# Kernel tuning notes

Measured on AMD Instinct MI355X. Metric: run time of the kernel, lower is better.

## Reference

```python
import jax, jax.numpy as jnp
import numpy as np

DIM = 512
NUM_HEADS = 8
HEAD_DIM = DIM // NUM_HEADS


def setup_inputs() -> dict:
    key = jax.random.key(0)
    k_x, k_qkv, k_p = jax.random.split(key, 3)
    b, n, c = 8, 4096, DIM
    x = jax.random.normal(k_x, (b, n, c), dtype=jnp.float32)
    # xavier_uniform for Linear(dim, 3*dim): limit = sqrt(6/(in+out))
    lim_qkv = float(np.sqrt(6.0 / (c + 3 * c)))
    w_qkv = jax.random.uniform(k_qkv, (c, 3 * c), dtype=jnp.float32, minval=-lim_qkv, maxval=lim_qkv)
    b_qkv = jnp.zeros((3 * c,), dtype=jnp.float32)
    lim_p = float(np.sqrt(6.0 / (c + c)))
    w_p = jax.random.uniform(k_p, (c, c), dtype=jnp.float32, minval=-lim_p, maxval=lim_p)
    b_p = jnp.zeros((c,), dtype=jnp.float32)
    temperature = jnp.full((NUM_HEADS, 1, 1), 1.0 / np.sqrt(HEAD_DIM), dtype=jnp.float32)
    return {"x": x, "w_qkv": w_qkv, "b_qkv": b_qkv, "w_p": w_p, "b_p": b_p,
            "temperature": temperature}


def reference(x, w_qkv, b_qkv, w_p, b_p, temperature):
    b, n, c = x.shape
    h, d = NUM_HEADS, HEAD_DIM
    qkv = x @ w_qkv + b_qkv                      # [b, n, 3c]
    q, k, v = jnp.split(qkv, 3, axis=-1)         # each [b, n, c]
    # -> [b, h, n, d]
    q = q.reshape(b, n, h, d).transpose(0, 2, 1, 3)
    k = k.reshape(b, n, h, d).transpose(0, 2, 1, 3)
    v = v.reshape(b, n, h, d).transpose(0, 2, 1, 3)
    # channel attention: d x d score matrix, reduced over tokens n
    scores = jnp.einsum('bhnd,bhne->bhde', q, k) * temperature  # [b,h,d,d]
    attn = jax.nn.softmax(scores, axis=-1)
    # y = attn @ v^T then permute -> [b, n, h, d]
    y = jnp.einsum('bhde,bhne->bnhd', attn, v).reshape(b, n, c)
    return y @ w_p + b_p
```

## Files before the change

kernel.cpp:

```cpp
#include <hip/hip_runtime.h>

typedef __attribute__((ext_vector_type(8))) short s16x8;
typedef __attribute__((ext_vector_type(4))) short s16x4;
typedef __attribute__((ext_vector_type(4))) float fx4;

__device__ inline unsigned short f2bf(float f) {
  unsigned u = __float_as_uint(f);
  u += 0x7fffu + ((u >> 16) & 1u);
  return (unsigned short)(u >> 16);
}
__device__ inline float bf2f(unsigned short s) {
  return __uint_as_float(((unsigned)s) << 16);
}

#define GLDS16(gp, lp) \
  __builtin_amdgcn_global_load_lds((const __attribute__((address_space(1))) void*)(gp), \
                                   (__attribute__((address_space(3))) void*)(lp), 16, 0, 0)

__global__ __launch_bounds__(256) void cast_x_k(const float* __restrict__ x,
                                                unsigned short* __restrict__ xb,
                                                unsigned short* __restrict__ xT,
                                                float* __restrict__ s_part) {
  __shared__ unsigned short lt[64 * 66];
  __shared__ float red[64 * 4];
  int blk = blockIdx.x;
  int b = blk >> 9, r = blk & 511, nt = r >> 3, ct = r & 7;
  int n0 = nt * 64, c0 = ct * 64;
  int t = threadIdx.x;
  int rn = t >> 2, seg = (t & 3) * 16;
  const float* xp = x + ((size_t)b * 4096 + n0 + rn) * 512 + c0 + seg;
  fx4 v0 = *(const fx4*)&xp[0], v1 = *(const fx4*)&xp[4];
  fx4 v2 = *(const fx4*)&xp[8], v3 = *(const fx4*)&xp[12];
  unsigned short h[16];
  h[0]=f2bf(v0[0]); h[1]=f2bf(v0[1]); h[2]=f2bf(v0[2]); h[3]=f2bf(v0[3]);
  h[4]=f2bf(v1[0]); h[5]=f2bf(v1[1]); h[6]=f2bf(v1[2]); h[7]=f2bf(v1[3]);
  h[8]=f2bf(v2[0]); h[9]=f2bf(v2[1]); h[10]=f2bf(v2[2]); h[11]=f2bf(v2[3]);
  h[12]=f2bf(v3[0]); h[13]=f2bf(v3[1]); h[14]=f2bf(v3[2]); h[15]=f2bf(v3[3]);
  unsigned short* xbo = xb + ((size_t)b * 4096 + n0 + rn) * 512 + c0 + seg;
  *(s16x8*)&xbo[0] = *(s16x8*)&h[0];
  *(s16x8*)&xbo[8] = *(s16x8*)&h[8];
#pragma unroll
  for (int k = 0; k < 16; ++k) lt[(seg + k) * 66 + rn] = h[k];
  __syncthreads();
  {
    int c = t & 63, q = t >> 6;
    float p = 0.f;
#pragma unroll
    for (int i = 0; i < 16; ++i) p += bf2f(lt[c * 66 + q * 16 + i]);
    red[c * 4 + q] = p;
  }
  __syncthreads();
  if (t < 64) {
    float s = red[t * 4] + red[t * 4 + 1] + red[t * 4 + 2] + red[t * 4 + 3];
    s_part[((size_t)(b * 64 + nt)) * 512 + c0 + t] = s;
  }
  int c = t >> 2, nseg = (t & 3) * 16;
  unsigned short* xto = xT + ((size_t)b * 512 + c0 + c) * 4096 + n0 + nseg;
  *(s16x8*)&xto[0] = *(s16x8*)&lt[c * 66 + nseg];
  *(s16x8*)&xto[8] = *(s16x8*)&lt[c * 66 + nseg + 8];
}

__global__ __launch_bounds__(256) void wk_t_k(const float* __restrict__ w,
                                              unsigned short* __restrict__ wkT) {
  __shared__ unsigned short lt[64 * 66];
  int blk = blockIdx.x;
  int rt = blk >> 3, ct = blk & 7;
  int t = threadIdx.x;
  int rn = t >> 2, seg = (t & 3) * 16;
  const float* wp = w + (size_t)(ct * 64 + rn) * 1536 + 512 + rt * 64 + seg;
#pragma unroll
  for (int k = 0; k < 16; ++k) lt[(seg + k) * 66 + rn] = f2bf(wp[k]);
  __syncthreads();
  int j = t >> 2, nseg = (t & 3) * 16;
  unsigned short* o = wkT + (size_t)(rt * 64 + j) * 512 + ct * 64 + nseg;
  *(s16x8*)&o[0] = *(s16x8*)&lt[j * 66 + nseg];
  *(s16x8*)&o[8] = *(s16x8*)&lt[j * 66 + nseg + 8];
}

__global__ __launch_bounds__(256) void wvwp_k(const float* __restrict__ w,
                                              const float* __restrict__ wp,
                                              unsigned short* __restrict__ wvb,
                                              unsigned short* __restrict__ wpb) {
  int blk = blockIdx.x, t = threadIdx.x;
  if (blk < 128) {
    int o = blk * 2048 + t * 8;
    int c = o >> 9, e = o & 511;
    const float* src = w + (size_t)c * 1536 + 1024 + e;
    unsigned short h[8];
#pragma unroll
    for (int i = 0; i < 8; ++i) h[i] = f2bf(src[i]);
    *(s16x8*)&wvb[o] = *(s16x8*)&h[0];
  } else {
    int o = (blk - 128) * 2048 + t * 8;
    unsigned short h[8];
#pragma unroll
    for (int i = 0; i < 8; ++i) h[i] = f2bf(wp[o + i]);
    *(s16x8*)&wpb[o] = *(s16x8*)&h[0];
  }
}

__global__ __launch_bounds__(256) void ub_k(const float* __restrict__ s_part,
                                            const float* __restrict__ w,
                                            float* __restrict__ u) {
  __shared__ float sb[512];
  int b = blockIdx.x >> 2, jq = blockIdx.x & 3;
  int t = threadIdx.x;
#pragma unroll
  for (int cc = 0; cc < 2; ++cc) {
    int c = cc * 256 + t;
    float a = 0.f;
    for (int nt = 0; nt < 64; ++nt)
      a += s_part[((size_t)(b * 64 + nt)) * 512 + c];
    sb[c] = a;
  }
  __syncthreads();
  int j = jq * 256 + t;
  float ua = 0.f;
  for (int c = 0; c < 512; ++c)
    ua += sb[c] * w[(size_t)c * 1536 + j];
  u[b * 1024 + j] = ua;
}

template <int MODE>
__global__ __launch_bounds__(256, 4) void gemm_k(
    const unsigned short* __restrict__ A0, const unsigned short* __restrict__ B0,
    const float* __restrict__ bias, unsigned short* __restrict__ obf,
    float* __restrict__ of32) {
  constexpr int LD = (MODE == 0) ? 4096 : 512;
  constexpr int KSTEPS = (MODE == 0) ? 32 : 16;
  constexpr int NWG = (MODE == 0) ? 512 : (MODE == 3) ? 1024 : 128;
  __shared__ alignas(16) unsigned short As[2][128 * 32];
  __shared__ alignas(16) unsigned short Bs[2][128 * 32];
  int tid = threadIdx.x, wave = tid >> 6, lane = tid & 63;
  int l15 = lane & 15, l16 = lane >> 4;
  int wr = wave >> 1, wc = wave & 1;

  int bid = (blockIdx.x & 7) * (NWG >> 3) + (blockIdx.x >> 3);
  int b = 0, mt = 0, nt = 0, ks = 0;
  if (MODE == 0) { ks = bid >> 7; int r = bid & 127; b = r >> 4; mt = (r >> 2) & 3; nt = r & 3; }
  else if (MODE == 3) { b = bid >> 7; int r = bid & 127; mt = r >> 2; nt = r & 3; }
  else { b = bid >> 4; mt = (bid >> 2) & 3; nt = bid & 3; }

  const unsigned short* Ab;
  const unsigned short* Bb;
  if (MODE == 0) { Ab = A0 + ((size_t)b * 512 + mt * 128) * 4096 + ks * 1024;
                   Bb = A0 + ((size_t)b * 512 + nt * 128) * 4096 + ks * 1024; }
  else if (MODE == 1) { Ab = A0 + (size_t)mt * 128 * 512;
                        Bb = B0 + ((size_t)b * 512 + nt * 128) * 512; }
  else if (MODE == 2) { Ab = A0 + ((size_t)b * 512 + mt * 128) * 512;
                        Bb = B0 + (size_t)nt * 128 * 512; }
  else { Ab = A0 + ((size_t)b * 4096 + mt * 128) * 512;
         Bb = B0 + ((size_t)b * 512 + nt * 128) * 512; }

  fx4 acc[4][4];
#pragma unroll
  for (int i = 0; i < 4; ++i)
#pragma unroll
    for (int j = 0; j < 4; ++j) acc[i][j] = (fx4){0.f, 0.f, 0.f, 0.f};

  int smr = wave * 16 + (lane >> 2);
  int skk = (((lane & 3) ^ ((lane >> 3) & 3))) * 8;
  const unsigned short* agp = Ab + (size_t)smr * LD + skk;
  const unsigned short* bgp = Bb + (size_t)smr * LD + skk;
  int ldsoff = wave * 512;

#define STAGE(buf, kt_)                                          \
  do {                                                           \
    int k0_ = (kt_) * 32;                                        \
    GLDS16(agp + k0_, &As[buf][ldsoff]);                         \
    GLDS16(agp + (size_t)64 * LD + k0_, &As[buf][ldsoff + 2048]);\
    GLDS16(bgp + k0_, &Bs[buf][ldsoff]);                         \
    GLDS16(bgp + (size_t)64 * LD + k0_, &Bs[buf][ldsoff + 2048]);\
  } while (0)

  STAGE(0, 0);
  asm volatile("s_waitcnt vmcnt(0)" ::: "memory");
  __builtin_amdgcn_s_barrier();

  int g = (l15 >> 1) & 3;
  int pa = (l16 ^ g) << 3;

  for (int kt = 0; kt < KSTEPS; ++kt) {
    int cur = kt & 1;
    if (kt < KSTEPS - 1) STAGE(cur ^ 1, kt + 1);

    s16x8 af[4], bf[4];
#pragma unroll
    for (int mi = 0; mi < 4; ++mi)
      af[mi] = *(const s16x8*)&As[cur][(wr * 64 + mi * 16 + l15) * 32 + pa];
#pragma unroll
    for (int nj = 0; nj < 4; ++nj)
      bf[nj] = *(const s16x8*)&Bs[cur][(wc * 64 + nj * 16 + l15) * 32 + pa];
#pragma unroll
    for (int mi = 0; mi < 4; ++mi)
#pragma unroll
      for (int nj = 0; nj < 4; ++nj)
        acc[mi][nj] = __builtin_amdgcn_mfma_f32_16x16x32_bf16(af[mi], bf[nj], acc[mi][nj], 0, 0, 0);

    asm volatile("s_waitcnt vmcnt(0)" ::: "memory");
    __builtin_amdgcn_s_barrier();
  }
#undef STAGE

  int R0 = mt * 128 + wr * 64, C0 = nt * 128 + wc * 64;
#pragma unroll
  for (int mi = 0; mi < 4; ++mi)
#pragma unroll
    for (int nj = 0; nj < 4; ++nj) {
      int gc = C0 + nj * 16 + l15;
#pragma unroll
      for (int r = 0; r < 4; ++r) {
        int gr = R0 + mi * 16 + l16 * 4 + r;
        float val = acc[mi][nj][r];
        if (MODE == 0) {
          of32[(((size_t)(ks * 8 + b)) * 512 + gr) * 512 + gc] = val;
        } else if (MODE == 1) {
          obf[((size_t)(b * 512 + gr)) * 512 + gc] = f2bf(val);
        } else if (MODE == 2) {
          obf[((size_t)(b * 512 + gr)) * 512 + gc] = f2bf(val);
        } else {
          of32[((size_t)(b * 4096 + gr)) * 512 + gc] = val + bias[b * 512 + gc];
        }
      }
    }
}

__global__ __launch_bounds__(256) void gsum_k(const float* __restrict__ Gpart,
                                              unsigned short* __restrict__ G16) {
  int i = (blockIdx.x * 256 + threadIdx.x) * 8;
  fx4 a0 = {0.f,0.f,0.f,0.f}, a1 = {0.f,0.f,0.f,0.f};
#pragma unroll
  for (int p = 0; p < 4; ++p) {
    a0 += *(const fx4*)&Gpart[(size_t)p * 2097152 + i];
    a1 += *(const fx4*)&Gpart[(size_t)p * 2097152 + i + 4];
  }
  unsigned short h[8];
  h[0]=f2bf(a0[0]); h[1]=f2bf(a0[1]); h[2]=f2bf(a0[2]); h[3]=f2bf(a0[3]);
  h[4]=f2bf(a1[0]); h[5]=f2bf(a1[1]); h[6]=f2bf(a1[2]); h[7]=f2bf(a1[3]);
  *(s16x8*)&G16[i] = *(s16x8*)&h[0];
}

__global__ __launch_bounds__(256) void s_k(const float* __restrict__ wq,
                                           const unsigned short* __restrict__ GWT,
                                           float* __restrict__ sp) {
  __shared__ alignas(16) float Ws[64 * 68];
  __shared__ alignas(16) float Gs[64 * 68];
  int bid = blockIdx.x;
  int bh = bid >> 3, cch = bid & 7;
  int b = bh >> 3, h = bh & 7;
  int t = threadIdx.x;
  int cr = t >> 2, sg = (t & 3) * 16;
  const float* wsrc = wq + (size_t)(cch * 64 + cr) * 1536 + h * 64 + sg;
#pragma unroll
  for (int kk = 0; kk < 16; ++kk) Ws[cr * 68 + sg + kk] = wsrc[kk];
  const unsigned short* gsrc = GWT + ((size_t)b * 512 + h * 64 + cr) * 512 + cch * 64 + sg;
#pragma unroll
  for (int kk = 0; kk < 16; ++kk) Gs[(sg + kk) * 68 + cr] = bf2f(gsrc[kk]);
  __syncthreads();
  int dg = t >> 4, eg = t & 15;
  float acc[4][4] = {{0.f}};
  for (int cc = 0; cc < 64; ++cc) {
    fx4 wv = *(const fx4*)&Ws[cc * 68 + dg * 4];
    fx4 pv = *(const fx4*)&Gs[cc * 68 + eg * 4];
#pragma unroll
    for (int i = 0; i < 4; ++i)
#pragma unroll
      for (int j = 0; j < 4; ++j) acc[i][j] += wv[i] * pv[j];
  }
  float* o = sp + (size_t)bid * 4096;
#pragma unroll
  for (int i = 0; i < 4; ++i)
#pragma unroll
    for (int j = 0; j < 4; ++j) o[(dg * 4 + i) * 64 + eg * 4 + j] = acc[i][j];
}

__global__ __launch_bounds__(256) void softmax_weff_k(
    const float* __restrict__ sp, const unsigned short* __restrict__ wpb,
    const float* __restrict__ temp, const float* __restrict__ b_qkv,
    const float* __restrict__ u, unsigned short* __restrict__ weffT) {
  __shared__ alignas(16) float S[64 * 64];
  __shared__ alignas(16) unsigned short wps[64 * 128];
  int bh = blockIdx.x >> 2, jblk = blockIdx.x & 3;
  int b = bh >> 3, h = bh & 7;
  int tid = threadIdx.x;
  float tval = temp[h];
  for (int i = tid * 4; i < 4096; i += 1024) {
    fx4 s = {0.f, 0.f, 0.f, 0.f};
    for (int seg = 0; seg < 8; ++seg)
      s += *(const fx4*)&sp[((size_t)(bh * 8 + seg)) * 4096 + i];
    int d = i >> 6, e0 = i & 63;
    float bq = b_qkv[h * 64 + d];
    float uq = u[b * 1024 + h * 64 + d];
#pragma unroll
    for (int jj = 0; jj < 4; ++jj) {
      int e = e0 + jj;
      float bk = b_qkv[512 + h * 64 + e];
      float ksum = u[b * 1024 + 512 + h * 64 + e] + 4096.0f * bk;
      s[jj] += bq * ksum + bk * uq;
    }
    s *= tval;
    *(fx4*)&S[i] = s;
  }
  for (int i = tid * 8; i < 8192; i += 2048) {
    int d = i >> 7, c = i & 127;
    *(s16x8*)&wps[i] = *(const s16x8*)&wpb[(size_t)(h * 64 + d) * 512 + jblk * 128 + c];
  }
  __syncthreads();
  if (tid < 64) {
    float* row = &S[tid * 64];
    float mx = row[0];
    for (int e = 1; e < 64; ++e) mx = fmaxf(mx, row[e]);
    float sum = 0.f;
    for (int e = 0; e < 64; ++e) { float p = __expf(row[e] - mx); row[e] = p; sum += p; }
    float inv = 1.f / sum;
    for (int e = 0; e < 64; ++e) row[e] *= inv;
  }
  __syncthreads();
  int jg = tid >> 4, eg = tid & 15;
  int j0 = jg * 8;
  float a[4][8];
#pragma unroll
  for (int i = 0; i < 4; ++i)
#pragma unroll
    for (int j = 0; j < 8; ++j) a[i][j] = 0.f;
  for (int d = 0; d < 64; ++d) {
    fx4 at = *(const fx4*)&S[d * 64 + eg * 4];
    s16x8 wv = *(const s16x8*)&wps[d * 128 + j0];
    float wf[8];
#pragma unroll
    for (int j = 0; j < 8; ++j) wf[j] = bf2f((unsigned short)wv[j]);
#pragma unroll
    for (int i = 0; i < 4; ++i)
#pragma unroll
      for (int j = 0; j < 8; ++j) a[i][j] += at[i] * wf[j];
  }
  int jglob = jblk * 128 + j0;
#pragma unroll
  for (int j = 0; j < 8; ++j) {
    unsigned short h4[4];
#pragma unroll
    for (int i = 0; i < 4; ++i) h4[i] = f2bf(a[i][j]);
    *(s16x4*)&weffT[(((size_t)b * 512 + jglob + j) << 9) + h * 64 + eg * 4] = *(s16x4*)&h4[0];
  }
}

__global__ __launch_bounds__(256) void bias2_k(const unsigned short* __restrict__ weffT,
                                               const float* __restrict__ b_qkv,
                                               const float* __restrict__ b_p,
                                               float* __restrict__ bias_out) {
  __shared__ float bv[512];
  int b = blockIdx.x;
  int t = threadIdx.x;
  bv[t] = b_qkv[1024 + t];
  bv[t + 256] = b_qkv[1280 + t];
  __syncthreads();
#pragma unroll
  for (int jj = 0; jj < 2; ++jj) {
    int j = jj * 256 + t;
    const unsigned short* wrow = &weffT[((size_t)(b * 512 + j)) << 9];
    float s = 0.f;
    for (int e = 0; e < 512; e += 8) {
      s16x8 v = *(const s16x8*)&wrow[e];
#pragma unroll
      for (int q = 0; q < 8; ++q) s += bv[e + q] * bf2f((unsigned short)v[q]);
    }
    bias_out[b * 512 + j] = b_p[j] + s;
  }
}

extern "C" void kernel_launch(void* const* d_in, const int* in_sizes, int n_in,
                              void* d_out, int out_size, void* d_ws, size_t ws_size,
                              hipStream_t stream) {
  const float* x      = (const float*)d_in[0];
  const float* w_qkv  = (const float*)d_in[1];
  const float* b_qkv  = (const float*)d_in[2];
  const float* w_p    = (const float*)d_in[3];
  const float* b_p    = (const float*)d_in[4];
  const float* temp   = (const float*)d_in[5];
  float* out = (float*)d_out;
  char* ws = (char*)d_ws;

  unsigned short* xb     = (unsigned short*)(ws + 0);
  unsigned short* xT     = (unsigned short*)(ws + 33554432);
  float*          Gpart  = (float*)(ws + 67108864);
  float*          s_part = (float*)(ws + 67108864);
  unsigned short* G16    = (unsigned short*)(ws + 100663296);
  unsigned short* GWT    = (unsigned short*)(ws + 104857600);
  float*          sp     = (float*)(ws + 109051904);
  unsigned short* wkT    = (unsigned short*)(ws + 117440512);
  unsigned short* wvb    = (unsigned short*)(ws + 117964800);
  unsigned short* wpb    = (unsigned short*)(ws + 118489088);
  float*          u      = (float*)(ws + 119013376);
  float*          bias_o = (float*)(ws + 119046144);
  unsigned short* weffT  = (unsigned short*)(ws + 33554432);
  unsigned short* wcombT = (unsigned short*)(ws + 37748736);

  cast_x_k<<<4096, 256, 0, stream>>>(x, xb, xT, s_part);
  wk_t_k<<<64, 256, 0, stream>>>(w_qkv, wkT);
  wvwp_k<<<256, 256, 0, stream>>>(w_qkv, w_p, wvb, wpb);
  ub_k<<<32, 256, 0, stream>>>(s_part, w_qkv, u);
  gemm_k<0><<<512, 256, 0, stream>>>(xT, nullptr, nullptr, nullptr, Gpart);
  gsum_k<<<1024, 256, 0, stream>>>(Gpart, G16);
  gemm_k<1><<<128, 256, 0, stream>>>(wkT, G16, nullptr, GWT, nullptr);
  s_k<<<512, 256, 0, stream>>>(w_qkv, GWT, sp);
  softmax_weff_k<<<256, 256, 0, stream>>>(sp, wpb, temp, b_qkv, u, weffT);
  bias2_k<<<8, 256, 0, stream>>>(weffT, b_qkv, b_p, bias_o);
  gemm_k<2><<<128, 256, 0, stream>>>(weffT, wvb, nullptr, wcombT, nullptr);
  gemm_k<3><<<1024, 256, 0, stream>>>(xb, wcombT, bias_o, nullptr, out);
}
```

Before: 167.3 us.

## Exploit Gram matrix symmetry and merge weight prep kernels

The split-K Gram GEMM X^T X now computes only the upper-triangular 128x128 tiles, 10 of 16 per batch and split. gsum_k rebuilds the lower-triangular blocks by transposing the matching upper partial sums through shared memory. Separately, the two weight-preparation kernels are merged into one launch. This cuts MMA work and Gpart traffic for the Gram step and removes one launch, at the cost of a transpose path in the reduction and a non-power-of-two tile mapping.

```diff
diff --git a/kernel.cpp b/kernel.cpp
--- a/kernel.cpp
+++ b/kernel.cpp
@@ -60,30 +60,26 @@
   *(s16x8*)&xto[8] = *(s16x8*)&lt[c * 66 + nseg + 8];
 }
 
-__global__ __launch_bounds__(256) void wk_t_k(const float* __restrict__ w,
-                                              unsigned short* __restrict__ wkT) {
+__global__ __launch_bounds__(256) void wprep_k(const float* __restrict__ w,
+                                               const float* __restrict__ wp,
+                                               unsigned short* __restrict__ wkT,
+                                               unsigned short* __restrict__ wvb,
+                                               unsigned short* __restrict__ wpb) {
   __shared__ unsigned short lt[64 * 66];
-  int blk = blockIdx.x;
-  int rt = blk >> 3, ct = blk & 7;
-  int t = threadIdx.x;
-  int rn = t >> 2, seg = (t & 3) * 16;
-  const float* wp = w + (size_t)(ct * 64 + rn) * 1536 + 512 + rt * 64 + seg;
-#pragma unroll
-  for (int k = 0; k < 16; ++k) lt[(seg + k) * 66 + rn] = f2bf(wp[k]);
-  __syncthreads();
-  int j = t >> 2, nseg = (t & 3) * 16;
-  unsigned short* o = wkT + (size_t)(rt * 64 + j) * 512 + ct * 64 + nseg;
-  *(s16x8*)&o[0] = *(s16x8*)&lt[j * 66 + nseg];
-  *(s16x8*)&o[8] = *(s16x8*)&lt[j * 66 + nseg + 8];
-}
-
-__global__ __launch_bounds__(256) void wvwp_k(const float* __restrict__ w,
-                                              const float* __restrict__ wp,
-                                              unsigned short* __restrict__ wvb,
-                                              unsigned short* __restrict__ wpb) {
   int blk = blockIdx.x, t = threadIdx.x;
-  if (blk < 128) {
-    int o = blk * 2048 + t * 8;
+  if (blk < 64) {
+    int rt = blk >> 3, ct = blk & 7;
+    int rn = t >> 2, seg = (t & 3) * 16;
+    const float* src = w + (size_t)(ct * 64 + rn) * 1536 + 512 + rt * 64 + seg;
+#pragma unroll
+    for (int k = 0; k < 16; ++k) lt[(seg + k) * 66 + rn] = f2bf(src[k]);
+    __syncthreads();
+    int j = t >> 2, nseg = (t & 3) * 16;
+    unsigned short* o = wkT + (size_t)(rt * 64 + j) * 512 + ct * 64 + nseg;
+    *(s16x8*)&o[0] = *(s16x8*)&lt[j * 66 + nseg];
+    *(s16x8*)&o[8] = *(s16x8*)&lt[j * 66 + nseg + 8];
+  } else if (blk < 192) {
+    int o = (blk - 64) * 2048 + t * 8;
     int c = o >> 9, e = o & 511;
     const float* src = w + (size_t)c * 1536 + 1024 + e;
     unsigned short h[8];
@@ -91,7 +87,7 @@
     for (int i = 0; i < 8; ++i) h[i] = f2bf(src[i]);
     *(s16x8*)&wvb[o] = *(s16x8*)&h[0];
   } else {
-    int o = (blk - 128) * 2048 + t * 8;
+    int o = (blk - 192) * 2048 + t * 8;
     unsigned short h[8];
 #pragma unroll
     for (int i = 0; i < 8; ++i) h[i] = f2bf(wp[o + i]);
@@ -128,7 +124,7 @@
     float* __restrict__ of32) {
   constexpr int LD = (MODE == 0) ? 4096 : 512;
   constexpr int KSTEPS = (MODE == 0) ? 32 : 16;
-  constexpr int NWG = (MODE == 0) ? 512 : (MODE == 3) ? 1024 : 128;
+  constexpr int NWG = (MODE == 0) ? 320 : (MODE == 3) ? 1024 : 128;
   __shared__ alignas(16) unsigned short As[2][128 * 32];
   __shared__ alignas(16) unsigned short Bs[2][128 * 32];
   int tid = threadIdx.x, wave = tid >> 6, lane = tid & 63;
@@ -137,7 +133,12 @@
 
   int bid = (blockIdx.x & 7) * (NWG >> 3) + (blockIdx.x >> 3);
   int b = 0, mt = 0, nt = 0, ks = 0;
-  if (MODE == 0) { ks = bid >> 7; int r = bid & 127; b = r >> 4; mt = (r >> 2) & 3; nt = r & 3; }
+  if (MODE == 0) {
+    const int TTM[10] = {0, 0, 0, 0, 1, 1, 1, 2, 2, 3};
+    const int TTN[10] = {0, 1, 2, 3, 1, 2, 3, 2, 3, 3};
+    ks = bid / 80; int r = bid - ks * 80; b = r / 10; int tt = r - b * 10;
+    mt = TTM[tt]; nt = TTN[tt];
+  }
   else if (MODE == 3) { b = bid >> 7; int r = bid & 127; mt = r >> 2; nt = r & 3; }
   else { b = bid >> 4; mt = (bid >> 2) & 3; nt = bid & 3; }
 
@@ -227,17 +228,46 @@
 
 __global__ __launch_bounds__(256) void gsum_k(const float* __restrict__ Gpart,
                                               unsigned short* __restrict__ G16) {
-  int i = (blockIdx.x * 256 + threadIdx.x) * 8;
-  fx4 a0 = {0.f,0.f,0.f,0.f}, a1 = {0.f,0.f,0.f,0.f};
-#pragma unroll
-  for (int p = 0; p < 4; ++p) {
-    a0 += *(const fx4*)&Gpart[(size_t)p * 2097152 + i];
-    a1 += *(const fx4*)&Gpart[(size_t)p * 2097152 + i + 4];
-  }
-  unsigned short h[8];
-  h[0]=f2bf(a0[0]); h[1]=f2bf(a0[1]); h[2]=f2bf(a0[2]); h[3]=f2bf(a0[3]);
-  h[4]=f2bf(a1[0]); h[5]=f2bf(a1[1]); h[6]=f2bf(a1[2]); h[7]=f2bf(a1[3]);
-  *(s16x8*)&G16[i] = *(s16x8*)&h[0];
+  __shared__ float ts[64 * 65];
+  int blk = blockIdx.x;
+  int b = blk >> 6, rt = (blk >> 3) & 7, ct = blk & 7;
+  int t = threadIdx.x;
+  int r0 = t >> 4, c0 = (t & 15) * 4;
+  bool lower = (rt >> 1) > (ct >> 1);
+  if (!lower) {
+#pragma unroll
+    for (int rr = 0; rr < 4; ++rr) {
+      int row = rr * 16 + r0;
+      size_t base = (((size_t)b * 512) + rt * 64 + row) * 512 + ct * 64 + c0;
+      fx4 a = {0.f, 0.f, 0.f, 0.f};
+#pragma unroll
+      for (int p = 0; p < 4; ++p) a += *(const fx4*)&Gpart[(size_t)p * 2097152 + base];
+      unsigned short h4[4];
+#pragma unroll
+      for (int i = 0; i < 4; ++i) h4[i] = f2bf(a[i]);
+      *(s16x4*)&G16[(((size_t)b * 512) + rt * 64 + row) * 512 + ct * 64 + c0] = *(s16x4*)&h4[0];
+    }
+  } else {
+#pragma unroll
+    for (int rr = 0; rr < 4; ++rr) {
+      int srow = rr * 16 + r0;
+      size_t base = (((size_t)b * 512) + ct * 64 + srow) * 512 + rt * 64 + c0;
+      fx4 a = {0.f, 0.f, 0.f, 0.f};
+#pragma unroll
+      for (int p = 0; p < 4; ++p) a += *(const fx4*)&Gpart[(size_t)p * 2097152 + base];
+#pragma unroll
+      for (int i = 0; i < 4; ++i) ts[(c0 + i) * 65 + srow] = a[i];
+    }
+    __syncthreads();
+#pragma unroll
+    for (int rr = 0; rr < 4; ++rr) {
+      int row = rr * 16 + r0;
+      unsigned short h4[4];
+#pragma unroll
+      for (int i = 0; i < 4; ++i) h4[i] = f2bf(ts[row * 65 + c0 + i]);
+      *(s16x4*)&G16[(((size_t)b * 512) + rt * 64 + row) * 512 + ct * 64 + c0] = *(s16x4*)&h4[0];
+    }
+  }
 }
 
 __global__ __launch_bounds__(256) void s_k(const float* __restrict__ wq,
@@ -396,11 +426,10 @@
   unsigned short* wcombT = (unsigned short*)(ws + 37748736);
 
   cast_x_k<<<4096, 256, 0, stream>>>(x, xb, xT, s_part);
-  wk_t_k<<<64, 256, 0, stream>>>(w_qkv, wkT);
-  wvwp_k<<<256, 256, 0, stream>>>(w_qkv, w_p, wvb, wpb);
+  wprep_k<<<320, 256, 0, stream>>>(w_qkv, w_p, wkT, wvb, wpb);
   ub_k<<<32, 256, 0, stream>>>(s_part, w_qkv, u);
-  gemm_k<0><<<512, 256, 0, stream>>>(xT, nullptr, nullptr, nullptr, Gpart);
-  gsum_k<<<1024, 256, 0, stream>>>(Gpart, G16);
+  gemm_k<0><<<320, 256, 0, stream>>>(xT, nullptr, nullptr, nullptr, Gpart);
+  gsum_k<<<512, 256, 0, stream>>>(Gpart, G16);
   gemm_k<1><<<128, 256, 0, stream>>>(wkT, G16, nullptr, GWT, nullptr);
   s_k<<<512, 256, 0, stream>>>(w_qkv, GWT, sp);
   softmax_weff_k<<<256, 256, 0, stream>>>(sp, wpb, temp, b_qkv, u, weffT);
```

New measurement: 166.0 us. No clear change (-0.8%).
